# Optimization experiments

Hardware: AMD Instinct MI355X
Metric: run time of the kernel (lower is better)

## Reference

```python
import jax, jax.numpy as jnp
import numpy as np

N_NODES = 100000
N_EDGES = 1600000
N_FEAT = 128
HIDDEN = 64
N_CLASSES = 40


def setup_inputs() -> dict:
    key = jax.random.key(0)
    ks = jax.random.split(key, 4)
    x = jax.random.normal(ks[0], (N_NODES, N_FEAT), dtype=jnp.float32)
    edge_index = jax.random.randint(ks[1], (2, N_EDGES), 0, N_NODES, dtype=jnp.int64)
    # Glorot-style init like PyG GCNConv
    W1 = jax.random.normal(ks[2], (N_FEAT, HIDDEN), dtype=jnp.float32) * (1.0 / np.sqrt(N_FEAT))
    b1 = jnp.zeros((HIDDEN,), dtype=jnp.float32)
    W2 = jax.random.normal(ks[3], (HIDDEN, N_CLASSES), dtype=jnp.float32) * (1.0 / np.sqrt(HIDDEN))
    b2 = jnp.zeros((N_CLASSES,), dtype=jnp.float32)
    return {"x": x, "edge_index": edge_index, "W1": W1, "b1": b1, "W2": W2, "b2": b2}


def _gcn_conv(x, src, dst, norm, W, b, n_nodes):
    # PyG GCNConv: transform first, then normalized scatter-add aggregation
    h = x @ W                                   # [N, out]
    msg = h[src] * norm[:, None]                # [E+N, out] gather
    out = jax.ops.segment_sum(msg, dst, num_segments=n_nodes)  # scatter-add
    return out + b


def _norm_and_loops(edge_index, n_nodes):
    # add self-loops, symmetric normalization deg^{-1/2} A_hat deg^{-1/2}
    loop = jnp.arange(n_nodes, dtype=edge_index.dtype)
    src = jnp.concatenate([edge_index[0], loop])
    dst = jnp.concatenate([edge_index[1], loop])
    deg = jax.ops.segment_sum(jnp.ones_like(dst, dtype=jnp.float32), dst, num_segments=n_nodes)
    dinv = jnp.where(deg > 0, jax.lax.rsqrt(jnp.maximum(deg, 1.0)), 0.0)
    norm = dinv[src] * dinv[dst]
    return src, dst, norm


def reference(x, edge_index, W1, b1, W2, b2):
    n_nodes = x.shape[0]
    src, dst, norm = _norm_and_loops(edge_index, n_nodes)
    h = _gcn_conv(x, src, dst, norm, W1, b1, n_nodes)
    h = jax.nn.relu(h)
    h = _gcn_conv(h, src, dst, norm, W2, b2, n_nodes)
    return jax.nn.log_softmax(h, axis=1)
```

## Files before the change

kernel.cpp:

```cpp
#include <hip/hip_runtime.h>
#include <hip/hip_bf16.h>
#include <string.h>

#define N_FEAT 128
#define HIDDEN 64
#define N_CLS  40
#define FILL_BLOCKS 1024
#define CHUNK_EDGES 16384
#define STAGE_CAP 6144
#define B_BITS 6
#define SRC_BITS 17

typedef __bf16 bf16x8 __attribute__((ext_vector_type(8)));
typedef float  f32x4  __attribute__((ext_vector_type(4)));

union Frag { unsigned u[4]; bf16x8 v; };

static __device__ inline int get_xcc() {
    return (int)(__builtin_amdgcn_s_getreg((3 << 11) | 20) & 7u);
}


static __device__ inline unsigned pack_bf16(float a, float b) {
    unsigned ba = __float_as_uint(a);
    unsigned bb = __float_as_uint(b);
    unsigned ra = (ba + 0x7fffu + ((ba >> 16) & 1u)) >> 16;
    unsigned rb = (bb + 0x7fffu + ((bb >> 16) & 1u)) >> 16;
    return (ra & 0xffffu) | (rb << 16);
}

static __device__ inline float2 unpack_bf16(unsigned v) {
    return make_float2(__uint_as_float(v << 16), __uint_as_float(v & 0xffff0000u));
}


__global__ void detect_layout_kernel(const int* __restrict__ ei, int* __restrict__ flag) {
    int lane = threadIdx.x;
    int v = ei[2 * lane + 1];
    unsigned long long b = __ballot(v != 0);
    if (lane == 0) flag[0] = (b == 0ull) ? 1 : 0;
}


__global__ __launch_bounds__(256) void bucket_hist_kernel(const int* __restrict__ ei,
                                                          const int* __restrict__ flag,
                                                          unsigned* __restrict__ bcnt,
                                                          int E, int nbuk) {
    __shared__ unsigned h[2048];
    for (int i = threadIdx.x; i < nbuk; i += 256) h[i] = 0u;
    __syncthreads();
    bool is64 = (flag[0] != 0);
    if (is64) {
        int idx = blockIdx.x * 256 + threadIdx.x;
        int stride2 = gridDim.x * 256 * 2;
        int Eeven = E & ~1;
        for (int e = idx * 2; e < Eeven; e += stride2) {
            uint4 dv = *(const uint4*)(ei + (size_t)2 * E + (size_t)2 * e);
            atomicAdd(&h[((int)dv.x) >> B_BITS], 1u);
            atomicAdd(&h[((int)dv.z) >> B_BITS], 1u);
        }
        for (int e = Eeven + idx; e < E; e += gridDim.x * 256) {
            int d = ei[(size_t)2 * E + (size_t)2 * e];
            atomicAdd(&h[d >> B_BITS], 1u);
        }
    } else {
        const int* dstp = ei + E;
        for (int e = blockIdx.x * 256 + threadIdx.x; e < E; e += gridDim.x * 256) {
            int d = dstp[e];
            atomicAdd(&h[d >> B_BITS], 1u);
        }
    }
    __syncthreads();
    for (int i = threadIdx.x; i < nbuk; i += 256)
        if (h[i]) atomicAdd(&bcnt[i], h[i]);
}


__global__ __launch_bounds__(512) void bucket_scan_kernel(const unsigned* __restrict__ bcnt,
                                                          unsigned* __restrict__ bbase,
                                                          unsigned* __restrict__ bcur, int nbuk) {
    __shared__ unsigned tmp[512];
    __shared__ unsigned carry;
    if (threadIdx.x == 0) carry = 0u;
    __syncthreads();
    for (int base = 0; base < nbuk; base += 512) {
        int i = base + threadIdx.x;
        unsigned v = (i < nbuk) ? bcnt[i] : 0u;
        tmp[threadIdx.x] = v;
        __syncthreads();
#pragma unroll
        for (int off = 1; off < 512; off <<= 1) {
            unsigned t = (threadIdx.x >= (unsigned)off) ? tmp[threadIdx.x - off] : 0u;
            __syncthreads();
            tmp[threadIdx.x] += t;
            __syncthreads();
        }
        unsigned excl = tmp[threadIdx.x] - v + carry;
        if (i < nbuk) {
            bbase[i] = excl;
            bcur[(size_t)i * 16] = excl;
        }
        __syncthreads();
        if (threadIdx.x == 511) carry += tmp[511];
        __syncthreads();
    }
}


__global__ __launch_bounds__(256) void fill_buckets_kernel(const int* __restrict__ ei,
                                                           const int* __restrict__ flag,
                                                           unsigned* __restrict__ bcur,
                                                           unsigned* __restrict__ ctr,
                                                           unsigned* __restrict__ tmpbuf,
                                                           int E, int nbuk) {
    int r = get_xcc();
    int bpx = (nbuk + 7) >> 3;
    int blo = r * bpx;
    int bhi = min(nbuk, blo + bpx);
    int nlb = bhi - blo;
    bool is64 = (flag[0] != 0);
    const size_t dstoff = (size_t)2 * E;

    __shared__ unsigned stage[STAGE_CAP];
    __shared__ unsigned hist[256], lbase[256], lcur[256];
    __shared__ unsigned tail_s, chunk_s;

    int lane = threadIdx.x & 63;
    unsigned long long lmask_lt = (lane == 0) ? 0ull : ((~0ull) >> (64 - lane));

    auto stage_edge = [&](bool own, unsigned v, unsigned lb) {
        unsigned long long mask = __ballot(own ? 1 : 0);
        int cnt = __popcll(mask);
        if (cnt) {
            unsigned bp = 0;
            int leader = __builtin_ctzll(mask);
            if (lane == leader) bp = atomicAdd(&tail_s, (unsigned)cnt);
            bp = __shfl(bp, leader);
            if (own) {
                unsigned pos = bp + (unsigned)__popcll(mask & lmask_lt);
                if (pos < STAGE_CAP) {
                    stage[pos] = v;
                    atomicAdd(&hist[lb], 1u);
                } else {
                    unsigned slot = __hip_atomic_fetch_add(&bcur[(size_t)(blo + (int)lb) * 16], 1u,
                                                           __ATOMIC_RELAXED, __HIP_MEMORY_SCOPE_WORKGROUP);
                    tmpbuf[slot] = v & 0x7fffffu;
                }
            }
        }
    };

    for (;;) {
        if (threadIdx.x == 0) {
            chunk_s = __hip_atomic_fetch_add(&ctr[r * 64], 1u, __ATOMIC_RELAXED,
                                             __HIP_MEMORY_SCOPE_WORKGROUP);
            tail_s = 0u;
        }
        if (threadIdx.x < 256) { hist[threadIdx.x] = 0u; lcur[threadIdx.x] = 0u; }
        __syncthreads();
        long long base = (long long)chunk_s * CHUNK_EDGES;
        if (base >= E) break;
        int end = (int)min((long long)E, base + CHUNK_EDGES);

        if (is64) {
            for (int e = (int)base + 2 * threadIdx.x; e + 1 < end; e += 512) {
                uint4 sv = *(const uint4*)(ei + (size_t)2 * e);
                uint4 dv = *(const uint4*)(ei + dstoff + (size_t)2 * e);
                {
                    int d = (int)dv.x;
                    int b = d >> B_BITS;
                    bool own = (b >= blo && b < bhi);
                    unsigned lb = own ? (unsigned)(b - blo) : 0u;
                    unsigned v = (lb << 23) | ((unsigned)(d & ((1 << B_BITS) - 1)) << SRC_BITS) | sv.x;
                    stage_edge(own, v, lb);
                }
                {
                    int d = (int)dv.z;
                    int b = d >> B_BITS;
                    bool own = (b >= blo && b < bhi);
                    unsigned lb = own ? (unsigned)(b - blo) : 0u;
                    unsigned v = (lb << 23) | ((unsigned)(d & ((1 << B_BITS) - 1)) << SRC_BITS) | sv.z;
                    stage_edge(own, v, lb);
                }
            }
            if ((end - (int)base) & 1) {
                bool own = false; unsigned v = 0, lb = 0;
                if (threadIdx.x == 0) {
                    int e = end - 1;
                    int d = ei[dstoff + (size_t)2 * e];
                    int b = d >> B_BITS;
                    if (b >= blo && b < bhi) {
                        own = true; lb = (unsigned)(b - blo);
                        v = (lb << 23) | ((unsigned)(d & ((1 << B_BITS) - 1)) << SRC_BITS)
                            | (unsigned)ei[(size_t)2 * e];
                    }
                }
                stage_edge(own, v, lb);
            }
        } else {
            for (int e = (int)base + threadIdx.x; e < end; e += 256) {
                int d = ei[(size_t)E + e];
                int b = d >> B_BITS;
                bool own = (b >= blo && b < bhi);
                unsigned lb = own ? (unsigned)(b - blo) : 0u;
                unsigned v = (lb << 23) | ((unsigned)(d & ((1 << B_BITS) - 1)) << SRC_BITS)
                             | (own ? (unsigned)ei[e] : 0u);
                stage_edge(own, v, lb);
            }
        }
        __syncthreads();

        for (int lb = threadIdx.x; lb < nlb; lb += 256) {
            unsigned h = hist[lb];
            if (h) lbase[lb] = __hip_atomic_fetch_add(&bcur[(size_t)(blo + lb) * 16], h,
                                                      __ATOMIC_RELAXED, __HIP_MEMORY_SCOPE_WORKGROUP);
        }
        __syncthreads();

        unsigned tl = min(tail_s, (unsigned)STAGE_CAP);
        for (unsigned i = threadIdx.x; i < tl; i += 256) {
            unsigned v = stage[i];
            unsigned lb = v >> 23;
            unsigned off = atomicAdd(&lcur[lb], 1u);
            tmpbuf[lbase[lb] + off] = v & 0x7fffffu;
        }
        __syncthreads();
    }
}


__global__ __launch_bounds__(256) void bucket_to_csr_kernel(const unsigned* __restrict__ tmpbuf,
                                                            const unsigned* __restrict__ bbase,
                                                            unsigned* __restrict__ deg,
                                                            unsigned* __restrict__ rowptr,
                                                            float* __restrict__ dinv,
                                                            int* __restrict__ csr_src,
                                                            int nbuk, int N, int E) {
    int b = blockIdx.x;
    int tid = threadIdx.x;
    unsigned beg = bbase[b];
    unsigned end = (b + 1 < nbuk) ? bbase[b + 1] : (unsigned)E;
    int d0 = b << B_BITS;
    const int ND = 1 << B_BITS;
    __shared__ unsigned hist[ND], scn[ND], cur[ND];
    if (tid < ND) { hist[tid] = 0u; cur[tid] = 0u; }
    __syncthreads();
    for (unsigned i = beg + tid; i < end; i += 256)
        atomicAdd(&hist[tmpbuf[i] >> SRC_BITS], 1u);
    __syncthreads();
    if (tid == 0) {
        unsigned run = 0;
        for (int k = 0; k < ND; ++k) { scn[k] = run; run += hist[k]; }
    }
    __syncthreads();
    if (tid < ND) {
        int d = d0 + tid;
        if (d < N) {
            unsigned dg = hist[tid];
            deg[d] = dg;
            dinv[d] = rsqrtf((float)(dg + 1u));
            rowptr[d] = beg + scn[tid];
        }
    }
    __syncthreads();
    for (unsigned i = beg + tid; i < end; i += 256) {
        unsigned v = tmpbuf[i];
        unsigned dl = v >> SRC_BITS;
        unsigned s = v & ((1u << SRC_BITS) - 1u);
        unsigned p = atomicAdd(&cur[dl], 1u);
        csr_src[beg + scn[dl] + p] = (int)s;
    }
}


__global__ __launch_bounds__(256) void gemm1_mfma_kernel(const float* __restrict__ x,
                                                         const float* __restrict__ W1,
                                                         unsigned* __restrict__ h1b, int N) {
    int lane = threadIdx.x & 63;
    int quad = lane >> 4;
    int col  = lane & 15;

    Frag B[4][4];
#pragma unroll
    for (int c = 0; c < 4; ++c)
#pragma unroll
        for (int ks = 0; ks < 4; ++ks) {
            int n = c * 16 + col;
#pragma unroll
            for (int jj = 0; jj < 4; ++jj) {
                int k = ks * 32 + quad * 8 + 2 * jj;
                B[c][ks].u[jj] = pack_bf16(W1[k * HIDDEN + n], W1[(k + 1) * HIDDEN + n]);
            }
        }

    int wave_id = blockIdx.x * 4 + (threadIdx.x >> 6);
    int nwaves  = gridDim.x * 4;
    int ntiles  = (N + 15) >> 4;

    for (int rt = wave_id; rt < ntiles; rt += nwaves) {
        int rowA = rt * 16 + col;
        Frag A[4];
#pragma unroll
        for (int ks = 0; ks < 4; ++ks) {
            float4 a0 = make_float4(0.f, 0.f, 0.f, 0.f), a1 = a0;
            if (rowA < N) {
                const float4* ap = (const float4*)(x + (size_t)rowA * N_FEAT + ks * 32 + quad * 8);
                a0 = ap[0];
                a1 = ap[1];
            }
            A[ks].u[0] = pack_bf16(a0.x, a0.y);
            A[ks].u[1] = pack_bf16(a0.z, a0.w);
            A[ks].u[2] = pack_bf16(a1.x, a1.y);
            A[ks].u[3] = pack_bf16(a1.z, a1.w);
        }
        f32x4 acc[4] = {{0.f, 0.f, 0.f, 0.f}, {0.f, 0.f, 0.f, 0.f},
                        {0.f, 0.f, 0.f, 0.f}, {0.f, 0.f, 0.f, 0.f}};
#pragma unroll
        for (int ks = 0; ks < 4; ++ks)
#pragma unroll
            for (int c = 0; c < 4; ++c)
                acc[c] = __builtin_amdgcn_mfma_f32_16x16x32_bf16(A[ks].v, B[c][ks].v, acc[c], 0, 0, 0);

        int rowD = rt * 16 + quad * 4;
#pragma unroll
        for (int c = 0; c < 4; ++c)
#pragma unroll
            for (int r = 0; r < 4; ++r) {
                float v = acc[c][r];
                float nxt = __shfl_down(v, 1);
                int row = rowD + r;
                if (((lane & 1) == 0) && row < N)
                    h1b[(size_t)row * 32 + ((c * 16 + col) >> 1)] = pack_bf16(v, nxt);
            }
    }
}


__global__ __launch_bounds__(256) void gemm2_mfma_kernel(const unsigned* __restrict__ actb,
                                                         const float* __restrict__ W2,
                                                         unsigned* __restrict__ h2a,
                                                         unsigned* __restrict__ h2c, int N) {
    int lane = threadIdx.x & 63;
    int quad = lane >> 4;
    int col  = lane & 15;

    Frag B[3][2];
#pragma unroll
    for (int c = 0; c < 3; ++c)
#pragma unroll
        for (int ks = 0; ks < 2; ++ks) {
            int n = c * 16 + col;
#pragma unroll
            for (int jj = 0; jj < 4; ++jj) {
                int k = ks * 32 + quad * 8 + 2 * jj;
                float w0 = (n < N_CLS) ? W2[k * N_CLS + n] : 0.f;
                float w1 = (n < N_CLS) ? W2[(k + 1) * N_CLS + n] : 0.f;
                B[c][ks].u[jj] = pack_bf16(w0, w1);
            }
        }

    int wave_id = blockIdx.x * 4 + (threadIdx.x >> 6);
    int nwaves  = gridDim.x * 4;
    int ntiles  = (N + 15) >> 4;

    for (int rt = wave_id; rt < ntiles; rt += nwaves) {
        int rowA = rt * 16 + col;
        Frag A[2];
#pragma unroll
        for (int ks = 0; ks < 2; ++ks) {
            uint4 u = make_uint4(0u, 0u, 0u, 0u);
            if (rowA < N)
                u = *(const uint4*)(actb + (size_t)rowA * 32 + ks * 16 + quad * 4);
            A[ks].u[0] = u.x; A[ks].u[1] = u.y; A[ks].u[2] = u.z; A[ks].u[3] = u.w;
        }
        f32x4 acc[3] = {{0.f, 0.f, 0.f, 0.f}, {0.f, 0.f, 0.f, 0.f}, {0.f, 0.f, 0.f, 0.f}};
#pragma unroll
        for (int ks = 0; ks < 2; ++ks)
#pragma unroll
            for (int c = 0; c < 3; ++c)
                acc[c] = __builtin_amdgcn_mfma_f32_16x16x32_bf16(A[ks].v, B[c][ks].v, acc[c], 0, 0, 0);

        int rowD = rt * 16 + quad * 4;
#pragma unroll
        for (int c = 0; c < 3; ++c)
#pragma unroll
            for (int r = 0; r < 4; ++r) {
                float v = acc[c][r];
                float nxt = __shfl_down(v, 1);
                int row = rowD + r;
                int pair = (c * 16 + col) >> 1;
                if (((lane & 1) == 0) && row < N) {
                    if (pair < 16)
                        h2a[(size_t)row * 16 + pair] = pack_bf16(v, nxt);
                    else if (pair < 20)
                        h2c[(size_t)row * 4 + (pair - 16)] = pack_bf16(v, nxt);
                }
            }
    }
}


__global__ __launch_bounds__(256) void agg1_kernel(const unsigned* __restrict__ h1b,
                                                   const int* __restrict__ csr_src,
                                                   const unsigned* __restrict__ rowptr,
                                                   const unsigned* __restrict__ deg,
                                                   const float* __restrict__ dinv,
                                                   const float* __restrict__ b1,
                                                   unsigned* __restrict__ actb, int N) {
    int wave = threadIdx.x >> 6, lane = threadIdx.x & 63;
    int sub = lane >> 5, j = lane & 31;
    int d = blockIdx.x * 4 + wave;
    if (d >= N) return;
    float dv = dinv[d];
    float acc0 = 0.f, acc1 = 0.f;
    if (sub == 0) {
        float2 v = unpack_bf16(h1b[(size_t)d * 32 + j]);
        acc0 = dv * v.x; acc1 = dv * v.y;
    }
    unsigned beg = rowptr[d];
    int len = (int)deg[d];
    int i = 0;
    for (; i + 8 <= len; i += 8) {
        int s0 = csr_src[beg + i + sub];
        int s1 = csr_src[beg + i + 2 + sub];
        int s2 = csr_src[beg + i + 4 + sub];
        int s3 = csr_src[beg + i + 6 + sub];
        float w0 = dinv[s0], w1 = dinv[s1], w2 = dinv[s2], w3 = dinv[s3];
        unsigned v0 = h1b[(size_t)s0 * 32 + j];
        unsigned v1 = h1b[(size_t)s1 * 32 + j];
        unsigned v2 = h1b[(size_t)s2 * 32 + j];
        unsigned v3 = h1b[(size_t)s3 * 32 + j];
        float2 a0 = unpack_bf16(v0), a1 = unpack_bf16(v1);
        float2 a2 = unpack_bf16(v2), a3 = unpack_bf16(v3);
        acc0 += w0 * a0.x + w1 * a1.x + w2 * a2.x + w3 * a3.x;
        acc1 += w0 * a0.y + w1 * a1.y + w2 * a2.y + w3 * a3.y;
    }
    for (; i + 4 <= len; i += 4) {
        int sA = csr_src[beg + i + sub];
        int sB = csr_src[beg + i + 2 + sub];
        float wA = dinv[sA], wB = dinv[sB];
        float2 a = unpack_bf16(h1b[(size_t)sA * 32 + j]);
        float2 b = unpack_bf16(h1b[(size_t)sB * 32 + j]);
        acc0 += wA * a.x + wB * b.x;
        acc1 += wA * a.y + wB * b.y;
    }
    for (; i < len; i += 2) {
        int e = i + sub;
        if (e < len) {
            int s = csr_src[beg + e];
            float w = dinv[s];
            float2 a = unpack_bf16(h1b[(size_t)s * 32 + j]);
            acc0 += w * a.x;
            acc1 += w * a.y;
        }
    }
    acc0 += __shfl_xor(acc0, 32);
    acc1 += __shfl_xor(acc1, 32);
    if (sub == 0) {
        float2 bb = ((const float2*)b1)[j];
        float r0 = fmaxf(acc0 * dv + bb.x, 0.f);
        float r1 = fmaxf(acc1 * dv + bb.y, 0.f);
        actb[(size_t)d * 32 + j] = pack_bf16(r0, r1);
    }
}


__global__ __launch_bounds__(256) void agg2_lsm_kernel(const unsigned* __restrict__ h2a,
                                                       const unsigned* __restrict__ h2c,
                                                       const int* __restrict__ csr_src,
                                                       const unsigned* __restrict__ rowptr,
                                                       const unsigned* __restrict__ deg,
                                                       const float* __restrict__ dinv,
                                                       const float* __restrict__ b2,
                                                       float* __restrict__ out, int N) {
    int wave = threadIdx.x >> 6, lane = threadIdx.x & 63;
    int sub = lane >> 5, j = lane & 31;
    bool act = (j < 20);
    const unsigned* tab;
    unsigned str;
    if (j < 16) { tab = h2a + j; str = 16u; }
    else        { tab = h2c + (j - 16); str = 4u; }
    int d = blockIdx.x * 4 + wave;
    if (d >= N) return;
    float dv = dinv[d];
    float acc0 = 0.f, acc1 = 0.f;
    if (sub == 0 && act) {
        float2 v = unpack_bf16(tab[(size_t)d * str]);
        acc0 = dv * v.x; acc1 = dv * v.y;
    }
    unsigned beg = rowptr[d];
    int len = (int)deg[d];
    int i = 0;
    for (; i + 8 <= len; i += 8) {
        int s0 = csr_src[beg + i + sub];
        int s1 = csr_src[beg + i + 2 + sub];
        int s2 = csr_src[beg + i + 4 + sub];
        int s3 = csr_src[beg + i + 6 + sub];
        float w0 = dinv[s0], w1 = dinv[s1], w2 = dinv[s2], w3 = dinv[s3];
        if (act) {
            float2 a0 = unpack_bf16(tab[(size_t)s0 * str]);
            float2 a1 = unpack_bf16(tab[(size_t)s1 * str]);
            float2 a2 = unpack_bf16(tab[(size_t)s2 * str]);
            float2 a3 = unpack_bf16(tab[(size_t)s3 * str]);
            acc0 += w0 * a0.x + w1 * a1.x + w2 * a2.x + w3 * a3.x;
            acc1 += w0 * a0.y + w1 * a1.y + w2 * a2.y + w3 * a3.y;
        }
    }
    for (; i + 4 <= len; i += 4) {
        int sA = csr_src[beg + i + sub];
        int sB = csr_src[beg + i + 2 + sub];
        float wA = dinv[sA], wB = dinv[sB];
        if (act) {
            float2 a = unpack_bf16(tab[(size_t)sA * str]);
            float2 b = unpack_bf16(tab[(size_t)sB * str]);
            acc0 += wA * a.x + wB * b.x;
            acc1 += wA * a.y + wB * b.y;
        }
    }
    for (; i < len; i += 2) {
        int e = i + sub;
        if (e < len && act) {
            int s = csr_src[beg + e];
            float w = dinv[s];
            float2 a = unpack_bf16(tab[(size_t)s * str]);
            acc0 += w * a.x;
            acc1 += w * a.y;
        }
    }
    acc0 += __shfl_xor(acc0, 32);
    acc1 += __shfl_xor(acc1, 32);
    float v0 = -1e30f, v1 = -1e30f;
    if (act) {
        float2 bb = ((const float2*)b2)[j];
        v0 = acc0 * dv + bb.x;
        v1 = acc1 * dv + bb.y;
    }
    float m = fmaxf(v0, v1);
#pragma unroll
    for (int off = 32; off > 0; off >>= 1)
        m = fmaxf(m, __shfl_xor(m, off));
    float ex = (act && sub == 0) ? (expf(v0 - m) + expf(v1 - m)) : 0.f;
#pragma unroll
    for (int off = 32; off > 0; off >>= 1)
        ex += __shfl_xor(ex, off);
    float ls = logf(ex);
    if (act && sub == 0) {
        float2* orow = (float2*)(out + (size_t)d * N_CLS);
        orow[j] = make_float2(v0 - m - ls, v1 - m - ls);
    }
}


static inline size_t align_up(size_t x) { return (x + 255) & ~(size_t)255; }

extern "C" void kernel_launch(void* const* d_in, const int* in_sizes, int n_in,
                              void* d_out, int out_size, void* d_ws, size_t ws_size,
                              hipStream_t stream) {
    const float* x  = (const float*)d_in[0];
    const int*   ei = (const int*)d_in[1];
    const float* W1 = (const float*)d_in[2];
    const float* b1 = (const float*)d_in[3];
    const float* W2 = (const float*)d_in[4];
    const float* b2 = (const float*)d_in[5];

    int N = in_sizes[0] / N_FEAT;
    int E = in_sizes[1] / 2;
    int nbuk = (N + (1 << B_BITS) - 1) >> B_BITS;

    char* ws = (char*)d_ws;
    int*      flag    = (int*)ws;       ws += 256;
    unsigned* ctrs    = (unsigned*)ws;  ws += 4096;
    unsigned* bcnt    = (unsigned*)ws;  ws += align_up((size_t)nbuk * 4);
    unsigned* bbase   = (unsigned*)ws;  ws += align_up((size_t)nbuk * 4);
    unsigned* bcur    = (unsigned*)ws;  ws += align_up((size_t)nbuk * 64);
    unsigned* deg     = (unsigned*)ws;  ws += align_up((size_t)N * 4);
    float*    dinv    = (float*)ws;     ws += align_up((size_t)N * 4);
    unsigned* rowptr  = (unsigned*)ws;  ws += align_up((size_t)N * 4);
    unsigned* tmpbuf  = (unsigned*)ws;  ws += align_up((size_t)E * 4);
    int*      csr_src = (int*)ws;       ws += align_up((size_t)E * 4);
    unsigned* h1b     = (unsigned*)ws;  ws += align_up((size_t)N * 32 * 4);
    unsigned* actb    = (unsigned*)ws;  ws += align_up((size_t)N * 32 * 4);
    unsigned* h2a     = (unsigned*)ws;  ws += align_up((size_t)N * 16 * 4);
    unsigned* h2c     = (unsigned*)ws;  ws += align_up((size_t)N * 4 * 4);

    hipMemsetAsync(ctrs, 0, 4096, stream);
    hipMemsetAsync(bcnt, 0, (size_t)nbuk * 4, stream);

    detect_layout_kernel<<<1, 64, 0, stream>>>(ei, flag);
    bucket_hist_kernel<<<256, 256, 0, stream>>>(ei, flag, bcnt, E, nbuk);
    bucket_scan_kernel<<<1, 512, 0, stream>>>(bcnt, bbase, bcur, nbuk);
    fill_buckets_kernel<<<FILL_BLOCKS, 256, 0, stream>>>(ei, flag, bcur, ctrs, tmpbuf, E, nbuk);
    bucket_to_csr_kernel<<<nbuk, 256, 0, stream>>>(tmpbuf, bbase, deg, rowptr, dinv, csr_src, nbuk, N, E);

    gemm1_mfma_kernel<<<512, 256, 0, stream>>>(x, W1, h1b, N);
    agg1_kernel<<<(N + 3) / 4, 256, 0, stream>>>(h1b, csr_src, rowptr, deg, dinv, b1, actb, N);

    gemm2_mfma_kernel<<<512, 256, 0, stream>>>(actb, W2, h2a, h2c, N);
    agg2_lsm_kernel<<<(N + 3) / 4, 256, 0, stream>>>(h2a, h2c, csr_src, rowptr, deg, dinv, b2, (float*)d_out, N);
}
```

Measured before the change: 324.3 us.

## Spread bucket histogram atomics over 8 copies, retune fill, unroll aggregation by 16

The bucket histogram now adds into eight replicated count arrays, chosen by block index, so fewer blocks contend on the same global atomic addresses. The scan sums the eight copies, and the two memsets are merged into one. The fill kernel launches twice as many blocks with a smaller staging capacity. Both aggregation kernels gain a 16-edge unrolled loop to keep more gathers in flight, at the cost of more registers and possibly lower occupancy.

```diff
diff --git a/kernel.cpp b/kernel.cpp
--- a/kernel.cpp
+++ b/kernel.cpp
@@ -5,9 +5,9 @@
 #define N_FEAT 128
 #define HIDDEN 64
 #define N_CLS  40
-#define FILL_BLOCKS 1024
+#define FILL_BLOCKS 2048
 #define CHUNK_EDGES 16384
-#define STAGE_CAP 6144
+#define STAGE_CAP 4096
 #define B_BITS 6
 #define SRC_BITS 17
 
@@ -44,7 +44,7 @@
 
 __global__ __launch_bounds__(256) void bucket_hist_kernel(const int* __restrict__ ei,
                                                           const int* __restrict__ flag,
-                                                          unsigned* __restrict__ bcnt,
+                                                          unsigned* __restrict__ bcnt8,
                                                           int E, int nbuk) {
     __shared__ unsigned h[2048];
     for (int i = threadIdx.x; i < nbuk; i += 256) h[i] = 0u;
@@ -71,12 +71,13 @@
         }
     }
     __syncthreads();
+    unsigned copy = (blockIdx.x & 7u) << 11;
     for (int i = threadIdx.x; i < nbuk; i += 256)
-        if (h[i]) atomicAdd(&bcnt[i], h[i]);
-}
-
-
-__global__ __launch_bounds__(512) void bucket_scan_kernel(const unsigned* __restrict__ bcnt,
+        if (h[i]) atomicAdd(&bcnt8[copy + i], h[i]);
+}
+
+
+__global__ __launch_bounds__(512) void bucket_scan_kernel(const unsigned* __restrict__ bcnt8,
                                                           unsigned* __restrict__ bbase,
                                                           unsigned* __restrict__ bcur, int nbuk) {
     __shared__ unsigned tmp[512];
@@ -85,7 +86,11 @@
     __syncthreads();
     for (int base = 0; base < nbuk; base += 512) {
         int i = base + threadIdx.x;
-        unsigned v = (i < nbuk) ? bcnt[i] : 0u;
+        unsigned v = 0u;
+        if (i < nbuk) {
+#pragma unroll
+            for (int c = 0; c < 8; ++c) v += bcnt8[(c << 11) + i];
+        }
         tmp[threadIdx.x] = v;
         __syncthreads();
 #pragma unroll
@@ -420,6 +425,34 @@
     unsigned beg = rowptr[d];
     int len = (int)deg[d];
     int i = 0;
+    for (; i + 16 <= len; i += 16) {
+        int s0 = csr_src[beg + i + sub];
+        int s1 = csr_src[beg + i + 2 + sub];
+        int s2 = csr_src[beg + i + 4 + sub];
+        int s3 = csr_src[beg + i + 6 + sub];
+        int s4 = csr_src[beg + i + 8 + sub];
+        int s5 = csr_src[beg + i + 10 + sub];
+        int s6 = csr_src[beg + i + 12 + sub];
+        int s7 = csr_src[beg + i + 14 + sub];
+        float w0 = dinv[s0], w1 = dinv[s1], w2 = dinv[s2], w3 = dinv[s3];
+        float w4 = dinv[s4], w5 = dinv[s5], w6 = dinv[s6], w7 = dinv[s7];
+        unsigned v0 = h1b[(size_t)s0 * 32 + j];
+        unsigned v1 = h1b[(size_t)s1 * 32 + j];
+        unsigned v2 = h1b[(size_t)s2 * 32 + j];
+        unsigned v3 = h1b[(size_t)s3 * 32 + j];
+        unsigned v4 = h1b[(size_t)s4 * 32 + j];
+        unsigned v5 = h1b[(size_t)s5 * 32 + j];
+        unsigned v6 = h1b[(size_t)s6 * 32 + j];
+        unsigned v7 = h1b[(size_t)s7 * 32 + j];
+        float2 a0 = unpack_bf16(v0), a1 = unpack_bf16(v1);
+        float2 a2 = unpack_bf16(v2), a3 = unpack_bf16(v3);
+        float2 a4 = unpack_bf16(v4), a5 = unpack_bf16(v5);
+        float2 a6 = unpack_bf16(v6), a7 = unpack_bf16(v7);
+        acc0 += w0 * a0.x + w1 * a1.x + w2 * a2.x + w3 * a3.x
+              + w4 * a4.x + w5 * a5.x + w6 * a6.x + w7 * a7.x;
+        acc1 += w0 * a0.y + w1 * a1.y + w2 * a2.y + w3 * a3.y
+              + w4 * a4.y + w5 * a5.y + w6 * a6.y + w7 * a7.y;
+    }
     for (; i + 8 <= len; i += 8) {
         int s0 = csr_src[beg + i + sub];
         int s1 = csr_src[beg + i + 2 + sub];
@@ -491,6 +524,32 @@
     unsigned beg = rowptr[d];
     int len = (int)deg[d];
     int i = 0;
+    for (; i + 16 <= len; i += 16) {
+        int s0 = csr_src[beg + i + sub];
+        int s1 = csr_src[beg + i + 2 + sub];
+        int s2 = csr_src[beg + i + 4 + sub];
+        int s3 = csr_src[beg + i + 6 + sub];
+        int s4 = csr_src[beg + i + 8 + sub];
+        int s5 = csr_src[beg + i + 10 + sub];
+        int s6 = csr_src[beg + i + 12 + sub];
+        int s7 = csr_src[beg + i + 14 + sub];
+        float w0 = dinv[s0], w1 = dinv[s1], w2 = dinv[s2], w3 = dinv[s3];
+        float w4 = dinv[s4], w5 = dinv[s5], w6 = dinv[s6], w7 = dinv[s7];
+        if (act) {
+            float2 a0 = unpack_bf16(tab[(size_t)s0 * str]);
+            float2 a1 = unpack_bf16(tab[(size_t)s1 * str]);
+            float2 a2 = unpack_bf16(tab[(size_t)s2 * str]);
+            float2 a3 = unpack_bf16(tab[(size_t)s3 * str]);
+            float2 a4 = unpack_bf16(tab[(size_t)s4 * str]);
+            float2 a5 = unpack_bf16(tab[(size_t)s5 * str]);
+            float2 a6 = unpack_bf16(tab[(size_t)s6 * str]);
+            float2 a7 = unpack_bf16(tab[(size_t)s7 * str]);
+            acc0 += w0 * a0.x + w1 * a1.x + w2 * a2.x + w3 * a3.x
+                  + w4 * a4.x + w5 * a5.x + w6 * a6.x + w7 * a7.x;
+            acc1 += w0 * a0.y + w1 * a1.y + w2 * a2.y + w3 * a3.y
+                  + w4 * a4.y + w5 * a5.y + w6 * a6.y + w7 * a7.y;
+        }
+    }
     for (; i + 8 <= len; i += 8) {
         int s0 = csr_src[beg + i + sub];
         int s1 = csr_src[beg + i + 2 + sub];
@@ -570,7 +629,7 @@
     char* ws = (char*)d_ws;
     int*      flag    = (int*)ws;       ws += 256;
     unsigned* ctrs    = (unsigned*)ws;  ws += 4096;
-    unsigned* bcnt    = (unsigned*)ws;  ws += align_up((size_t)nbuk * 4);
+    unsigned* bcnt8   = (unsigned*)ws;  ws += 8 * 2048 * 4;
     unsigned* bbase   = (unsigned*)ws;  ws += align_up((size_t)nbuk * 4);
     unsigned* bcur    = (unsigned*)ws;  ws += align_up((size_t)nbuk * 64);
     unsigned* deg     = (unsigned*)ws;  ws += align_up((size_t)N * 4);
@@ -583,12 +642,11 @@
     unsigned* h2a     = (unsigned*)ws;  ws += align_up((size_t)N * 16 * 4);
     unsigned* h2c     = (unsigned*)ws;  ws += align_up((size_t)N * 4 * 4);
 
-    hipMemsetAsync(ctrs, 0, 4096, stream);
-    hipMemsetAsync(bcnt, 0, (size_t)nbuk * 4, stream);
+    hipMemsetAsync(ctrs, 0, 4096 + 8 * 2048 * 4, stream);
 
     detect_layout_kernel<<<1, 64, 0, stream>>>(ei, flag);
-    bucket_hist_kernel<<<256, 256, 0, stream>>>(ei, flag, bcnt, E, nbuk);
-    bucket_scan_kernel<<<1, 512, 0, stream>>>(bcnt, bbase, bcur, nbuk);
+    bucket_hist_kernel<<<256, 256, 0, stream>>>(ei, flag, bcnt8, E, nbuk);
+    bucket_scan_kernel<<<1, 512, 0, stream>>>(bcnt8, bbase, bcur, nbuk);
     fill_buckets_kernel<<<FILL_BLOCKS, 256, 0, stream>>>(ei, flag, bcur, ctrs, tmpbuf, E, nbuk);
     bucket_to_csr_kernel<<<nbuk, 256, 0, stream>>>(tmpbuf, bbase, deg, rowptr, dinv, csr_src, nbuk, N, E);
 
```

Measured after the change: 310.8 us. 4.2% less time.
